# Kernel optimization log

Measured on AMD Instinct MI355X. Metric: run time of the kernel, lower is better.

## Reference

```python
import jax, jax.numpy as jnp
import numpy as np

# Model hyperparameters (match init_kwargs)
S = 1000        # num_simulations
D = 16          # num_lca_dim
T = 3000        # num_time_steps
THRESHOLD = 1.0
LEAK = 0.1
COMPETITION = 0.1
SELF_EXC = 0.0
NOISE = 1.0
DT = 0.01
SQRT_STEP = float(np.sqrt(0.001))  # LCALayer hardcodes sqrt(0.001) regardless of time_step_size


def setup_inputs() -> dict:
    key = jax.random.key(0)
    ff_input = jax.random.normal(key, (S, D), dtype=jnp.float32)
    return {"ff_input": ff_input}


def reference(ff_input):
    eye = jnp.eye(D, dtype=ff_input.dtype)
    # gamma: off-diagonal = competition, diagonal = -self_excitation
    gamma = COMPETITION * (1.0 - eye) - SELF_EXC * eye
    keys = jax.random.split(jax.random.key(42), T)

    def step(carry, k):
        pre, act = carry
        # accumulators stop integrating once any unit crosses threshold
        active = jnp.all(jnp.abs(act) < THRESHOLD, axis=1, keepdims=True).astype(pre.dtype)
        pre = pre + (ff_input - LEAK * pre - act @ gamma) * active * DT
        dw = jax.random.normal(k, act.shape, dtype=pre.dtype) * (active * NOISE)
        pre = pre + dw * SQRT_STEP
        act = jax.nn.relu(pre)
        return (pre, act), (pre, act)

    init = (jnp.zeros((S, D), jnp.float32), jnp.zeros((S, D), jnp.float32))
    _, (pre_seq, act_seq) = jax.lax.scan(step, init, keys)  # [T, S, D]

    z = jnp.zeros((S, D, 1), jnp.float32)
    pre_all = jnp.concatenate([z, jnp.transpose(pre_seq, (1, 2, 0))], axis=2)  # [S, D, T+1]
    act_all = jnp.concatenate([z, jnp.transpose(act_seq, (1, 2, 0))], axis=2)  # [S, D, T+1]
    return pre_all, act_all
```

## Files before the change

### kernel.cpp

```cpp
#include <hip/hip_runtime.h>
#include <cstdint>

#define T_STEPS 3000
#define S_SIMS  1000
#define D_DIM   16
#define NJ      (S_SIMS * D_DIM)
#define ROW     (T_STEPS + 1)
#define HALF_OUT ((long long)NJ * ROW)

#define NPROD 7
#define DEPTH 32
#define BATCH 8
#define SQSTEP 0.03162277660168379f

__device__ uint2  g_keys[T_STEPS];
__device__ int    g_tf[S_SIMS];
__device__ float  g_ws_pre[(size_t)T_STEPS * NJ];

__device__ __forceinline__ uint32_t rotl32(uint32_t v, uint32_t d) {
  return (v << d) | (v >> (32u - d));
}

__device__ __forceinline__ void threefry2x32(uint32_t k0, uint32_t k1,
                                             uint32_t& x0, uint32_t& x1) {
  uint32_t k2 = k0 ^ k1 ^ 0x1BD11BDAu;
  x0 += k0; x1 += k1;
#define TFR(r) { x0 += x1; x1 = rotl32(x1, r); x1 ^= x0; }
  TFR(13u) TFR(15u) TFR(26u) TFR(6u)
  x0 += k1; x1 += k2 + 1u;
  TFR(17u) TFR(29u) TFR(16u) TFR(24u)
  x0 += k2; x1 += k0 + 2u;
  TFR(13u) TFR(15u) TFR(26u) TFR(6u)
  x0 += k0; x1 += k1 + 3u;
  TFR(17u) TFR(29u) TFR(16u) TFR(24u)
  x0 += k1; x1 += k2 + 4u;
  TFR(13u) TFR(15u) TFR(26u) TFR(6u)
  x0 += k2; x1 += k0 + 5u;
#undef TFR
}

__device__ __forceinline__ float bits_to_normal(uint32_t bits) {
  uint32_t fb = (bits >> 9) | 0x3f800000u;
  float f = __uint_as_float(fb) - 1.0f;
  const float lo = -0.99999994f;
  float u = f * 2.0f + lo;
  u = fmaxf(lo, u);

  float w = -0.6931471805599453f * __log2f((1.0f - u) * (1.0f + u));
  float p;
  if (w < 5.0f) {
    w = w - 2.5f;
    p = 2.81022636e-08f;
    p = fmaf(p, w, 3.43273939e-07f);
    p = fmaf(p, w, -3.5233877e-06f);
    p = fmaf(p, w, -4.39150654e-06f);
    p = fmaf(p, w, 0.00021858087f);
    p = fmaf(p, w, -0.00125372503f);
    p = fmaf(p, w, -0.00417768164f);
    p = fmaf(p, w, 0.246640727f);
    p = fmaf(p, w, 1.50140941f);
  } else {
    w = sqrtf(w) - 3.0f;
    p = -0.000200214257f;
    p = fmaf(p, w, 0.000100950558f);
    p = fmaf(p, w, 0.00134934322f);
    p = fmaf(p, w, -0.00367342844f);
    p = fmaf(p, w, 0.00573950773f);
    p = fmaf(p, w, -0.0076224613f);
    p = fmaf(p, w, 0.00943887047f);
    p = fmaf(p, w, 1.00167406f);
    p = fmaf(p, w, 2.83297682f);
  }
  return 1.41421356237f * (p * u);
}

__device__ __forceinline__ float noise_at(int t, int j) {
  uint2 k = g_keys[t];
  uint32_t x0 = 0u, x1 = (uint32_t)j;
  threefry2x32(k.x, k.y, x0, x1);
  return bits_to_normal(x0 ^ x1);
}

__global__ void keys_kernel() {
  int t = blockIdx.x * blockDim.x + threadIdx.x;
  if (t >= T_STEPS) return;
  uint32_t x0 = 0u, x1 = (uint32_t)t;
  threefry2x32(0u, 42u, x0, x1);
  g_keys[t] = make_uint2(x0, x1);
}

template <int CTRL>
__device__ __forceinline__ float dpp_movf(float v) {
  return __int_as_float(
      __builtin_amdgcn_update_dpp(0, __float_as_int(v), CTRL, 0xF, 0xF, true));
}
__device__ __forceinline__ float row16_sum(float a) {
  float s = a;
  s += dpp_movf<0xB1>(s);
  s += dpp_movf<0x4E>(s);
  s += dpp_movf<0x124>(s);
  s += dpp_movf<0x128>(s);
  return s;
}
__device__ __forceinline__ float row16_max(float a) {
  float m = a;
  m = fmaxf(m, dpp_movf<0xB1>(m));
  m = fmaxf(m, dpp_movf<0x4E>(m));
  m = fmaxf(m, dpp_movf<0x124>(m));
  m = fmaxf(m, dpp_movf<0x128>(m));
  return m;
}

__global__ __launch_bounds__(512) void sim_kernel(const float* __restrict__ ff) {
  __shared__ float sh_nbuf[DEPTH][64];
  __shared__ volatile unsigned sh_prodc[NPROD];
  __shared__ volatile unsigned sh_cons;
  __shared__ volatile unsigned sh_done;

  const int lane = threadIdx.x & 63;
  const int wid  = threadIdx.x >> 6;
  const int j    = blockIdx.x * 64 + lane;

  if (threadIdx.x < NPROD) sh_prodc[threadIdx.x] = 0u;
  if (threadIdx.x == 0) { sh_cons = 0u; sh_done = 0u; }
  __syncthreads();

  if (wid == 0) {
    const float ffv = ff[j];
    float pre = 0.0f, act = 0.0f;
    bool dead = false;
    int my_tf = T_STEPS;
    unsigned Rc = 0;

#define ENSURE(x)                                                     \
    while (Rc <= (unsigned)(x)) {                                     \
      unsigned mn = 0xffffffffu;                                      \
      for (int p_ = 0; p_ < NPROD; ++p_) {                            \
        unsigned lim = (unsigned)p_ + (unsigned)NPROD * sh_prodc[p_]; \
        if (lim < mn) mn = lim;                                       \
      }                                                               \
      Rc = mn;                                                        \
      if (Rc <= (unsigned)(x)) __builtin_amdgcn_s_sleep(2);           \
    }

    float n[BATCH], nn[BATCH], a[BATCH];
    ENSURE(BATCH - 1);
#pragma unroll
    for (int k = 0; k < BATCH; ++k) n[k] = sh_nbuf[k][lane];

    int t0 = 0;
    while (true) {
      if (lane == 0) sh_cons = (unsigned)(t0 + BATCH);
      const bool more = (t0 + BATCH < T_STEPS);
      if (more) {
        ENSURE(t0 + 2 * BATCH - 1);
#pragma unroll
        for (int k = 0; k < BATCH; ++k)
          nn[k] = sh_nbuf[(t0 + BATCH + k) & (DEPTH - 1)][lane];
      }

      float bmax = 0.0f;
      float* __restrict__ wsp = &g_ws_pre[(size_t)t0 * NJ + j];
#pragma unroll
      for (int k = 0; k < BATCH; ++k) {
        float s  = row16_sum(act);
        float q  = s - act;
        float e1 = fmaf(-0.1f, pre, ffv);
        float e2 = fmaf(-0.1f, q, e1);
        pre = fmaf(e2, 0.01f, pre);
        pre = fmaf(n[k], SQSTEP, pre);
        act = fmaxf(pre, 0.0f);
        a[k] = act;
        bmax = fmaxf(bmax, act);
        wsp[(size_t)k * NJ] = pre;
      }

      if (__any(bmax >= 1.0f)) {
        bool found = dead;
#pragma unroll
        for (int k = 0; k < BATCH; ++k) {
          float m = row16_max(a[k]);
          if (!found && m >= 1.0f) { found = true; my_tf = t0 + k + 1; }
        }
        if (found && !dead) {
          dead = true;
          pre = -1e30f;
          act = 0.0f;
        }
        if (__all(dead)) break;
      }

      if (!more) break;
#pragma unroll
      for (int k = 0; k < BATCH; ++k) n[k] = nn[k];
      t0 += BATCH;
    }
#undef ENSURE
    if ((lane & 15) == 0) g_tf[j >> 4] = my_tf;
    if (threadIdx.x == 0) sh_done = 1u;
  } else {
    const int p = wid - 1;
    unsigned count = 0;
    for (int t = p; t < T_STEPS; t += NPROD) {
      float n = noise_at(t, j);
      if (t >= DEPTH) {
        bool quit = false;
        while (true) {
          if (sh_done) { quit = true; break; }
          unsigned pc = sh_cons;
          if ((unsigned)t <= pc + (DEPTH - 1)) break;
          __builtin_amdgcn_s_sleep(8);
        }
        if (quit) break;
      }
      sh_nbuf[t & (DEPTH - 1)][lane] = n;
      asm volatile("s_waitcnt lgkmcnt(0)" ::: "memory");
      ++count;
      if (lane == 0) sh_prodc[p] = count;
    }
  }
}

__global__ __launch_bounds__(256) void fill_kernel(float* __restrict__ out) {
  const int j = blockIdx.x;
  const int tf = g_tf[j >> 4];
  float* __restrict__ pre_out = out + (size_t)j * ROW;
  float* __restrict__ act_out = out + HALF_OUT + (size_t)j * ROW;

  for (int idx = threadIdx.x; idx < ROW; idx += 256) {
    float v;
    if (idx == 0) {
      v = 0.0f;
    } else {
      int te = idx - 1;
      if (te > tf - 1) te = tf - 1;
      v = g_ws_pre[(size_t)te * NJ + j];
    }
    pre_out[idx] = v;
    act_out[idx] = fmaxf(v, 0.0f);
  }
}

extern "C" void kernel_launch(void* const* d_in, const int* in_sizes, int n_in,
                              void* d_out, int out_size, void* d_ws, size_t ws_size,
                              hipStream_t stream) {
  const float* ff = (const float*)d_in[0];
  float* out = (float*)d_out;

  keys_kernel<<<dim3((T_STEPS + 255) / 256), dim3(256), 0, stream>>>();
  sim_kernel<<<dim3(NJ / 64), dim3(512), 0, stream>>>(ff);
  fill_kernel<<<dim3(NJ), dim3(256), 0, stream>>>(out);
}
```

Before: 133.2 us.

## Fuse simulation and output fill into one persistent kernel with per-sim flags

Merges the sim and fill kernels into one persistent kernel. Spare blocks, and sim blocks once they finish, pull output rows from an atomic work counter and wait on per-simulation release flags. The output fill can then overlap the tail of slow simulations instead of waiting for the whole sim grid. It also skips workspace writes after a simulation stops, raises the consumer wave's priority, and shortens the producer sleep. The cost is a dependence on all blocks being co-resident, since spinning waiters could otherwise deadlock, plus one small wave per row doing the fill, which may lower store throughput.

```diff
diff --git a/kernel.cpp b/kernel.cpp
--- a/kernel.cpp
+++ b/kernel.cpp
@@ -8,19 +8,21 @@
 #define ROW     (T_STEPS + 1)
 #define HALF_OUT ((long long)NJ * ROW)
 
-#define NPROD 7
-#define DEPTH 32
-#define BATCH 8
+#define NSIMB  250
+#define GRID   384
+#define NPROD  7
+#define DEPTH  32
+#define BATCH  8
 #define SQSTEP 0.03162277660168379f
 
-__device__ uint2  g_keys[T_STEPS];
-__device__ int    g_tf[S_SIMS];
-__device__ float  g_ws_pre[(size_t)T_STEPS * NJ];
+__device__ uint2    g_keys[T_STEPS];
+__device__ int      g_tf_pub[S_SIMS];
+__device__ unsigned g_c1;
+__device__ float    g_ws_pre[(size_t)T_STEPS * NJ];
 
 __device__ __forceinline__ uint32_t rotl32(uint32_t v, uint32_t d) {
   return (v << d) | (v >> (32u - d));
 }
-
 __device__ __forceinline__ void threefry2x32(uint32_t k0, uint32_t k1,
                                              uint32_t& x0, uint32_t& x1) {
   uint32_t k2 = k0 ^ k1 ^ 0x1BD11BDAu;
@@ -45,7 +47,6 @@
   const float lo = -0.99999994f;
   float u = f * 2.0f + lo;
   u = fmaxf(lo, u);
-
   float w = -0.6931471805599453f * __log2f((1.0f - u) * (1.0f + u));
   float p;
   if (w < 5.0f) {
@@ -81,12 +82,15 @@
   return bits_to_normal(x0 ^ x1);
 }
 
-__global__ void keys_kernel() {
-  int t = blockIdx.x * blockDim.x + threadIdx.x;
-  if (t >= T_STEPS) return;
-  uint32_t x0 = 0u, x1 = (uint32_t)t;
-  threefry2x32(0u, 42u, x0, x1);
-  g_keys[t] = make_uint2(x0, x1);
+__global__ void init_kernel() {
+  int i = blockIdx.x * blockDim.x + threadIdx.x;
+  if (i < T_STEPS) {
+    uint32_t x0 = 0u, x1 = (uint32_t)i;
+    threefry2x32(0u, 42u, x0, x1);
+    g_keys[i] = make_uint2(x0, x1);
+  }
+  if (i < S_SIMS) g_tf_pub[i] = -1;
+  if (i == 0) g_c1 = 0u;
 }
 
 template <int CTRL>
@@ -111,133 +115,157 @@
   return m;
 }
 
-__global__ __launch_bounds__(512) void sim_kernel(const float* __restrict__ ff) {
+__global__ __launch_bounds__(512) void fused_kernel(const float* __restrict__ ff,
+                                                    float* __restrict__ out) {
   __shared__ float sh_nbuf[DEPTH][64];
   __shared__ volatile unsigned sh_prodc[NPROD];
   __shared__ volatile unsigned sh_cons;
   __shared__ volatile unsigned sh_done;
 
-  const int lane = threadIdx.x & 63;
-  const int wid  = threadIdx.x >> 6;
-  const int j    = blockIdx.x * 64 + lane;
-
-  if (threadIdx.x < NPROD) sh_prodc[threadIdx.x] = 0u;
-  if (threadIdx.x == 0) { sh_cons = 0u; sh_done = 0u; }
-  __syncthreads();
-
-  if (wid == 0) {
-    const float ffv = ff[j];
-    float pre = 0.0f, act = 0.0f;
-    bool dead = false;
-    int my_tf = T_STEPS;
-    unsigned Rc = 0;
+  const int tid  = threadIdx.x;
+  const int lane = tid & 63;
+  const int wid  = tid >> 6;
+
+  if (blockIdx.x < NSIMB) {
+    if (tid < NPROD) sh_prodc[tid] = 0u;
+    if (tid == 0) { sh_cons = 0u; sh_done = 0u; }
+    __syncthreads();
+    const int j = blockIdx.x * 64 + lane;
+
+    if (wid == 0) {
+      __builtin_amdgcn_s_setprio(1);
+      const float ffv = ff[j];
+      float pre = 0.0f, act = 0.0f;
+      bool dead = false;
+      unsigned Rc = 0;
 
 #define ENSURE(x)                                                     \
-    while (Rc <= (unsigned)(x)) {                                     \
-      unsigned mn = 0xffffffffu;                                      \
-      for (int p_ = 0; p_ < NPROD; ++p_) {                            \
-        unsigned lim = (unsigned)p_ + (unsigned)NPROD * sh_prodc[p_]; \
-        if (lim < mn) mn = lim;                                       \
-      }                                                               \
-      Rc = mn;                                                        \
-      if (Rc <= (unsigned)(x)) __builtin_amdgcn_s_sleep(2);           \
+      while (Rc <= (unsigned)(x)) {                                   \
+        unsigned mn = 0xffffffffu;                                    \
+        for (int p_ = 0; p_ < NPROD; ++p_) {                          \
+          unsigned lim = (unsigned)p_ + (unsigned)NPROD * sh_prodc[p_]; \
+          if (lim < mn) mn = lim;                                     \
+        }                                                             \
+        Rc = mn;                                                      \
+        if (Rc <= (unsigned)(x)) __builtin_amdgcn_s_sleep(2);         \
+      }
+
+      float n[BATCH], nn[BATCH], a[BATCH];
+      ENSURE(BATCH - 1);
+#pragma unroll
+      for (int k = 0; k < BATCH; ++k) n[k] = sh_nbuf[k][lane];
+
+      int t0 = 0;
+      while (true) {
+        if (lane == 0) sh_cons = (unsigned)(t0 + BATCH);
+        const bool more = (t0 + BATCH < T_STEPS);
+        if (more) {
+          ENSURE(t0 + 2 * BATCH - 1);
+#pragma unroll
+          for (int k = 0; k < BATCH; ++k)
+            nn[k] = sh_nbuf[(t0 + BATCH + k) & (DEPTH - 1)][lane];
+        }
+
+        float bmax = 0.0f;
+        float* __restrict__ wsp = g_ws_pre + (size_t)t0 * NJ + j;
+#pragma unroll
+        for (int k = 0; k < BATCH; ++k) {
+          float s  = row16_sum(act);
+          float e1 = fmaf(-0.1f, pre, ffv);
+          float e2 = fmaf(-0.1f, s - act, e1);
+          pre = fmaf(e2, 0.01f, pre);
+          pre = fmaf(n[k], SQSTEP, pre);
+          act = fmaxf(pre, 0.0f);
+          a[k] = act;
+          bmax = fmaxf(bmax, act);
+          if (!dead) wsp[(size_t)k * NJ] = pre;
+        }
+
+        if (__any(bmax >= 1.0f)) {
+          bool found = dead;
+          int ctf = 0;
+#pragma unroll
+          for (int k = 0; k < BATCH; ++k) {
+            float m = row16_max(a[k]);
+            if (!found && m >= 1.0f) { found = true; ctf = t0 + k + 1; }
+          }
+          if (found && !dead) {
+            dead = true;
+            pre = -1e30f;
+            act = 0.0f;
+            if ((lane & 15) == 0)
+              __hip_atomic_store(&g_tf_pub[j >> 4], ctf,
+                                 __ATOMIC_RELEASE, __HIP_MEMORY_SCOPE_AGENT);
+          }
+          if (__all(dead)) break;
+        }
+
+        if (!more) break;
+#pragma unroll
+        for (int k = 0; k < BATCH; ++k) n[k] = nn[k];
+        t0 += BATCH;
+      }
+#undef ENSURE
+      if (!dead && (lane & 15) == 0)
+        __hip_atomic_store(&g_tf_pub[j >> 4], T_STEPS,
+                           __ATOMIC_RELEASE, __HIP_MEMORY_SCOPE_AGENT);
+      if (lane == 0) sh_done = 1u;
+      __builtin_amdgcn_s_setprio(0);
+    } else {
+      const int p = wid - 1;
+      unsigned count = 0;
+      bool quit = false;
+      for (int t = p; t < T_STEPS; t += NPROD) {
+        if (sh_done) break;
+        float nv = noise_at(t, j);
+        if (t >= DEPTH) {
+          while (true) {
+            if (sh_done) { quit = true; break; }
+            unsigned pc = sh_cons;
+            if ((unsigned)t <= pc + (DEPTH - 1)) break;
+            __builtin_amdgcn_s_sleep(4);
+          }
+          if (quit) break;
+        }
+        sh_nbuf[t & (DEPTH - 1)][lane] = nv;
+        asm volatile("s_waitcnt lgkmcnt(0)" ::: "memory");
+        ++count;
+        if (lane == 0) sh_prodc[p] = count;
+      }
     }
-
-    float n[BATCH], nn[BATCH], a[BATCH];
-    ENSURE(BATCH - 1);
-#pragma unroll
-    for (int k = 0; k < BATCH; ++k) n[k] = sh_nbuf[k][lane];
-
-    int t0 = 0;
-    while (true) {
-      if (lane == 0) sh_cons = (unsigned)(t0 + BATCH);
-      const bool more = (t0 + BATCH < T_STEPS);
-      if (more) {
-        ENSURE(t0 + 2 * BATCH - 1);
-#pragma unroll
-        for (int k = 0; k < BATCH; ++k)
-          nn[k] = sh_nbuf[(t0 + BATCH + k) & (DEPTH - 1)][lane];
-      }
-
-      float bmax = 0.0f;
-      float* __restrict__ wsp = &g_ws_pre[(size_t)t0 * NJ + j];
-#pragma unroll
-      for (int k = 0; k < BATCH; ++k) {
-        float s  = row16_sum(act);
-        float q  = s - act;
-        float e1 = fmaf(-0.1f, pre, ffv);
-        float e2 = fmaf(-0.1f, q, e1);
-        pre = fmaf(e2, 0.01f, pre);
-        pre = fmaf(n[k], SQSTEP, pre);
-        act = fmaxf(pre, 0.0f);
-        a[k] = act;
-        bmax = fmaxf(bmax, act);
-        wsp[(size_t)k * NJ] = pre;
-      }
-
-      if (__any(bmax >= 1.0f)) {
-        bool found = dead;
-#pragma unroll
-        for (int k = 0; k < BATCH; ++k) {
-          float m = row16_max(a[k]);
-          if (!found && m >= 1.0f) { found = true; my_tf = t0 + k + 1; }
-        }
-        if (found && !dead) {
-          dead = true;
-          pre = -1e30f;
-          act = 0.0f;
-        }
-        if (__all(dead)) break;
-      }
-
-      if (!more) break;
-#pragma unroll
-      for (int k = 0; k < BATCH; ++k) n[k] = nn[k];
-      t0 += BATCH;
+  }
+
+  while (true) {
+    unsigned i = 0;
+    if (lane == 0) i = atomicAdd(&g_c1, 1u);
+    i = (unsigned)__shfl((int)i, 0);
+    if (i >= NJ) break;
+    const int j = (int)((i * 997u) % (unsigned)NJ);
+    const int s = j >> 4;
+
+    int tf = __hip_atomic_load(&g_tf_pub[s], __ATOMIC_RELAXED,
+                               __HIP_MEMORY_SCOPE_AGENT);
+    while (tf < 0) {
+      __builtin_amdgcn_s_sleep(8);
+      tf = __hip_atomic_load(&g_tf_pub[s], __ATOMIC_RELAXED,
+                             __HIP_MEMORY_SCOPE_AGENT);
     }
-#undef ENSURE
-    if ((lane & 15) == 0) g_tf[j >> 4] = my_tf;
-    if (threadIdx.x == 0) sh_done = 1u;
-  } else {
-    const int p = wid - 1;
-    unsigned count = 0;
-    for (int t = p; t < T_STEPS; t += NPROD) {
-      float n = noise_at(t, j);
-      if (t >= DEPTH) {
-        bool quit = false;
-        while (true) {
-          if (sh_done) { quit = true; break; }
-          unsigned pc = sh_cons;
-          if ((unsigned)t <= pc + (DEPTH - 1)) break;
-          __builtin_amdgcn_s_sleep(8);
-        }
-        if (quit) break;
-      }
-      sh_nbuf[t & (DEPTH - 1)][lane] = n;
-      asm volatile("s_waitcnt lgkmcnt(0)" ::: "memory");
-      ++count;
-      if (lane == 0) sh_prodc[p] = count;
+    (void)__hip_atomic_load(&g_tf_pub[s], __ATOMIC_ACQUIRE,
+                            __HIP_MEMORY_SCOPE_AGENT);
+
+    float* __restrict__ pre_out = out + (size_t)j * ROW;
+    float* __restrict__ act_out = pre_out + HALF_OUT;
+    const float vlast = g_ws_pre[(size_t)(tf - 1) * NJ + j];
+    for (int idx = lane; idx < ROW; idx += 64) {
+      float v = 0.0f;
+      if (idx > 0) {
+        int te = idx - 1;
+        v = vlast;
+        if (te < tf) v = g_ws_pre[(size_t)te * NJ + j];
+      }
+      pre_out[idx] = v;
+      act_out[idx] = fmaxf(v, 0.0f);
     }
-  }
-}
-
-__global__ __launch_bounds__(256) void fill_kernel(float* __restrict__ out) {
-  const int j = blockIdx.x;
-  const int tf = g_tf[j >> 4];
-  float* __restrict__ pre_out = out + (size_t)j * ROW;
-  float* __restrict__ act_out = out + HALF_OUT + (size_t)j * ROW;
-
-  for (int idx = threadIdx.x; idx < ROW; idx += 256) {
-    float v;
-    if (idx == 0) {
-      v = 0.0f;
-    } else {
-      int te = idx - 1;
-      if (te > tf - 1) te = tf - 1;
-      v = g_ws_pre[(size_t)te * NJ + j];
-    }
-    pre_out[idx] = v;
-    act_out[idx] = fmaxf(v, 0.0f);
   }
 }
 
@@ -247,7 +275,6 @@
   const float* ff = (const float*)d_in[0];
   float* out = (float*)d_out;
 
-  keys_kernel<<<dim3((T_STEPS + 255) / 256), dim3(256), 0, stream>>>();
-  sim_kernel<<<dim3(NJ / 64), dim3(512), 0, stream>>>(ff);
-  fill_kernel<<<dim3(NJ), dim3(256), 0, stream>>>(out);
-}
+  init_kernel<<<dim3(16), dim3(256), 0, stream>>>();
+  fused_kernel<<<dim3(GRID), dim3(512), 0, stream>>>(ff, out);
+}
```

Measured after the change: 286.9 us. 115% more time.
